# Kernel tuning notes

Hardware: AMD Instinct MI355X
Metric: run time of the kernel (lower is better)

The kernel has to match this reference:

```python
import jax, jax.numpy as jnp
import numpy as np

B, S, H = 32, 2048, 1024


def sparsemax(z, axis):
    # Martins & Astudillo (2016) sparsemax projection onto the simplex.
    n = z.shape[axis]
    z_sorted = -jnp.sort(-z, axis=axis)  # descending sort
    z_cum = jnp.cumsum(z_sorted, axis=axis)
    k = jnp.arange(1, n + 1, dtype=z.dtype).reshape(
        [n if i == (axis % z.ndim) else 1 for i in range(z.ndim)])
    support = (1.0 + k * z_sorted) > z_cum
    k_z = jnp.sum(support, axis=axis, keepdims=True)  # support size per row
    tau = (jnp.take_along_axis(z_cum, k_z.astype(jnp.int32) - 1, axis=axis) - 1.0) / k_z.astype(z.dtype)
    return jnp.maximum(z - tau, 0.0)


def setup_inputs() -> dict:
    key = jax.random.key(0)
    ks = jax.random.split(key, 8)
    s = 1.0 / np.sqrt(H)
    return {
        "encoder_output": jax.random.normal(ks[0], (B, S, H), jnp.float32),
        "decoder_hidden": jax.random.normal(ks[1], (B, H), jnp.float32),
        "Wa_w": jax.random.uniform(ks[2], (H, H), jnp.float32, -s, s),
        "Wa_b": jax.random.uniform(ks[3], (H,), jnp.float32, -s, s),
        "Ua_w": jax.random.uniform(ks[4], (H, H), jnp.float32, -s, s),
        "Ua_b": jax.random.uniform(ks[5], (H,), jnp.float32, -s, s),
        "Va_w": jax.random.uniform(ks[6], (1, H), jnp.float32, -s, s),
        "Va_b": jax.random.uniform(ks[7], (1,), jnp.float32, -s, s),
    }


def reference(encoder_output, decoder_hidden, Wa_w, Wa_b, Ua_w, Ua_b, Va_w, Va_b):
    # query: [B, 1, H]
    query = (decoder_hidden @ Wa_w.T + Wa_b)[:, None, :]
    # keys: [B, S, H]
    keys = jnp.einsum('bsh,oh->bso', encoder_output, Ua_w) + Ua_b
    # energy: [B, S]
    energy = jnp.einsum('bsh,h->bs', jnp.tanh(keys + query), Va_w[0]) + Va_b[0]
    attention_weights = sparsemax(energy, axis=1)  # [B, S]
    # context: [B, 1, H]
    context = jnp.einsum('bs,bsh->bh', attention_weights, encoder_output)[:, None, :]
    return (context, attention_weights)
```

## Files before the change

kernel.cpp:

```cpp
#include <hip/hip_runtime.h>
#include <stdint.h>
#include <stddef.h>

#define BB 32
#define SS 2048
#define HH 1024
#define MTOT (BB*SS)
#define NC 16

typedef _Float16 h8 __attribute__((ext_vector_type(8)));
typedef float f32x4 __attribute__((ext_vector_type(4)));

__device__ __forceinline__ void gload_lds16(const void* g, void* l) {
  __builtin_amdgcn_global_load_lds(
      (const __attribute__((address_space(1))) void*)g,
      (__attribute__((address_space(3))) void*)l,
      16, 0, 0);
}

__device__ __forceinline__ float fast_tanh(float x) {
  x = fminf(15.f, fmaxf(-15.f, x));
  float t = __expf(2.f * x);
  return (t - 1.f) * __builtin_amdgcn_rcpf(t + 1.f);
}

__global__ __launch_bounds__(256) void cvt_h(const float* __restrict__ src,
                                             _Float16* __restrict__ dst) {
  int t = blockIdx.x * 256 + threadIdx.x;
  const float4* s4 = (const float4*)src + (size_t)t * 2;
  float4 f0 = s4[0], f1 = s4[1];
  h8 v;
  v[0]=(_Float16)f0.x; v[1]=(_Float16)f0.y; v[2]=(_Float16)f0.z; v[3]=(_Float16)f0.w;
  v[4]=(_Float16)f1.x; v[5]=(_Float16)f1.y; v[6]=(_Float16)f1.z; v[7]=(_Float16)f1.w;
  *(h8*)(dst + (size_t)t * 8) = v;
}

__global__ __launch_bounds__(256) void query_k(const float* __restrict__ dh,
                                               const float* __restrict__ Wa,
                                               const float* __restrict__ Wa_b,
                                               const float* __restrict__ Ua_b,
                                               float* __restrict__ qv) {
  int gw = (blockIdx.x * 256 + threadIdx.x) >> 6;
  int lane = threadIdx.x & 63;
  int o = gw >> 5;
  int b = gw & 31;
  const float4* x4 = (const float4*)(dh + (size_t)b * HH);
  const float4* w4 = (const float4*)(Wa + (size_t)o * HH);
  float s = 0.f;
#pragma unroll
  for (int j = 0; j < 4; ++j) {
    float4 a = x4[lane + 64 * j];
    float4 c = w4[lane + 64 * j];
    s += a.x * c.x + a.y * c.y + a.z * c.z + a.w * c.w;
  }
#pragma unroll
  for (int d = 32; d >= 1; d >>= 1) s += __shfl_xor(s, d, 64);
  if (lane == 0) qv[b * HH + o] = s + Wa_b[o] + Ua_b[o];
}

template<bool AH>
__global__ __launch_bounds__(256) void energy_gemm(const float* __restrict__ Ag,
                                                   const _Float16* __restrict__ Ahp,
                                                   const _Float16* __restrict__ Bh,
                                                   const float* __restrict__ qv,
                                                   const float* __restrict__ Va,
                                                   float* __restrict__ energy) {
  __shared__ __align__(16) _Float16 As[128 * 64];
  __shared__ __align__(16) _Float16 Bs[128 * 64];

  const int tid  = threadIdx.x;
  const int lane = tid & 63;
  const int w    = tid >> 6;
  const int wrow = (w & 1) * 64;
  const int wcol = (w >> 1) * 64;
  const int lr   = lane & 15;
  const int lq   = lane >> 4;

  const int x     = blockIdx.x;
  const int xcd   = x & 7;
  const int i6    = x >> 3;
  const int strip = xcd * 64 + (i6 >> 3);
  const int nblk  = i6 & 7;
  const int m0    = strip * 128;
  const int n0    = nblk * 128;

  f32x4 acc[4][4];
#pragma unroll
  for (int i = 0; i < 4; ++i)
#pragma unroll
    for (int j = 0; j < 4; ++j) acc[i][j] = (f32x4){0.f, 0.f, 0.f, 0.f};

  for (int kt = 0; kt < 16; ++kt) {
    const int k0 = kt * 64;
#pragma unroll
    for (int i = 0; i < 4; ++i) {
      int g = tid + 256 * i;
      int r = g >> 3;
      int c = (g & 7) ^ (r & 7);
      gload_lds16(Bh + (size_t)(n0 + r) * HH + k0 + c * 8, &Bs[g * 8]);
    }
    if constexpr (AH) {
#pragma unroll
      for (int i = 0; i < 4; ++i) {
        int g = tid + 256 * i;
        int r = g >> 3;
        int c = (g & 7) ^ (r & 7);
        gload_lds16(Ahp + (size_t)(m0 + r) * HH + k0 + c * 8, &As[g * 8]);
      }
    } else {
      float4 fa[8];
#pragma unroll
      for (int i = 0; i < 4; ++i) {
        int g = tid + 256 * i;
        int r = g >> 3;
        int c = (g & 7) ^ (r & 7);
        const float* src = Ag + (size_t)(m0 + r) * HH + k0 + c * 8;
        fa[2 * i]     = *(const float4*)src;
        fa[2 * i + 1] = *(const float4*)(src + 4);
      }
#pragma unroll
      for (int i = 0; i < 4; ++i) {
        int g = tid + 256 * i;
        h8 v;
        v[0]=(_Float16)fa[2*i].x;   v[1]=(_Float16)fa[2*i].y;
        v[2]=(_Float16)fa[2*i].z;   v[3]=(_Float16)fa[2*i].w;
        v[4]=(_Float16)fa[2*i+1].x; v[5]=(_Float16)fa[2*i+1].y;
        v[6]=(_Float16)fa[2*i+1].z; v[7]=(_Float16)fa[2*i+1].w;
        *(h8*)&As[g * 8] = v;
      }
    }
    __syncthreads();
#pragma unroll
    for (int kk = 0; kk < 2; ++kk) {
      h8 af[4], bf[4];
#pragma unroll
      for (int i = 0; i < 4; ++i) {
        int ra = wrow + i * 16 + lr;
        int ca = kk * 4 + lq;
        af[i] = *(const h8*)&As[(ra * 8 + (ca ^ (ra & 7))) * 8];
        int rb = wcol + i * 16 + lr;
        bf[i] = *(const h8*)&Bs[(rb * 8 + (ca ^ (rb & 7))) * 8];
      }
#pragma unroll
      for (int i = 0; i < 4; ++i)
#pragma unroll
        for (int j = 0; j < 4; ++j)
          acc[i][j] = __builtin_amdgcn_mfma_f32_16x16x32_f16(af[i], bf[j], acc[i][j], 0, 0, 0);
    }
    __syncthreads();
  }

  const int bq = m0 >> 11;
  float qvv[4], vaw[4];
#pragma unroll
  for (int j = 0; j < 4; ++j) {
    int n = n0 + wcol + j * 16 + lr;
    qvv[j] = qv[bq * HH + n];
    vaw[j] = Va[n];
  }
#pragma unroll
  for (int i = 0; i < 4; ++i) {
    float p[4] = {0.f, 0.f, 0.f, 0.f};
#pragma unroll
    for (int j = 0; j < 4; ++j)
#pragma unroll
      for (int r = 0; r < 4; ++r)
        p[r] += fast_tanh(acc[i][j][r] + qvv[j]) * vaw[j];
#pragma unroll
    for (int r = 0; r < 4; ++r) {
      float v = p[r];
      v += __shfl_xor(v, 1, 64);
      v += __shfl_xor(v, 2, 64);
      v += __shfl_xor(v, 4, 64);
      v += __shfl_xor(v, 8, 64);
      if (lr == 0) {
        int m = m0 + wrow + i * 16 + lq * 4 + r;
        atomicAdd(&energy[m], v);
      }
    }
  }
}

__global__ __launch_bounds__(256) void sparse_k(const float* __restrict__ energy,
                                                const float* __restrict__ Va_b,
                                                float* __restrict__ attn,
                                                int* __restrict__ scnt,
                                                int* __restrict__ ssidx,
                                                float* __restrict__ saval) {
  const int b = blockIdx.x;
  const int tid = threadIdx.x;
  const int lane = tid & 63;
  const int w = tid >> 6;
  __shared__ int cnt;
  if (tid == 0) cnt = 0;

  const float* z = energy + (size_t)b * SS;
  const float vb = Va_b[0];
  float zv[32];
#pragma unroll
  for (int k = 0; k < 32; ++k) zv[k] = z[lane + 64 * k] + vb;

  float mx = zv[0];
#pragma unroll
  for (int k = 1; k < 32; ++k) mx = fmaxf(mx, zv[k]);
#pragma unroll
  for (int d = 32; d >= 1; d >>= 1) mx = fmaxf(mx, __shfl_xor(mx, d, 64));

  float lo = mx - 1.f, hi = mx;
  for (int it = 0; it < 40; ++it) {
    float tau = 0.5f * (lo + hi);
    float ss = 0.f;
#pragma unroll
    for (int k = 0; k < 32; ++k) ss += fmaxf(zv[k] - tau, 0.f);
#pragma unroll
    for (int d = 32; d >= 1; d >>= 1) ss += __shfl_xor(ss, d, 64);
    if (ss >= 1.f) lo = tau; else hi = tau;
  }
  const float tau = 0.5f * (lo + hi);

  __syncthreads();
  int* si = ssidx + b * SS;
  float* av = saval + b * SS;
#pragma unroll
  for (int kk = 0; kk < 8; ++kk) {
    int k = w * 8 + kk;
    int s = lane + 64 * k;
    float a = fmaxf(zv[k] - tau, 0.f);
    attn[(size_t)b * SS + s] = a;
    if (a > 0.f) {
      int p = atomicAdd(&cnt, 1);
      si[p] = s;
      av[p] = a;
    }
  }
  __syncthreads();
  if (tid == 0) scnt[b] = cnt;
}

__global__ __launch_bounds__(256) void ctx_k(const float* __restrict__ enc,
                                             const int* __restrict__ scnt,
                                             const int* __restrict__ ssidx,
                                             const float* __restrict__ saval,
                                             float* __restrict__ ctx) {
  const int b = blockIdx.x >> 4;
  const int c = blockIdx.x & (NC - 1);
  const int tid = threadIdx.x;
  const int n = scnt[b];
  if (c >= n) return;

  const float* eb = enc + (size_t)b * SS * HH;
  const int* si = ssidx + b * SS;
  const float* av = saval + b * SS;

  float c0 = 0.f, c1 = 0.f, c2 = 0.f, c3 = 0.f;
  for (int p = c; p < n; p += NC) {
    float a = av[p];
    const float* row = eb + (size_t)si[p] * HH;
    c0 += a * row[tid];
    c1 += a * row[tid + 256];
    c2 += a * row[tid + 512];
    c3 += a * row[tid + 768];
  }
  atomicAdd(&ctx[(size_t)b * HH + tid],       c0);
  atomicAdd(&ctx[(size_t)b * HH + tid + 256], c1);
  atomicAdd(&ctx[(size_t)b * HH + tid + 512], c2);
  atomicAdd(&ctx[(size_t)b * HH + tid + 768], c3);
}

extern "C" void kernel_launch(void* const* d_in, const int* in_sizes, int n_in,
                              void* d_out, int out_size, void* d_ws, size_t ws_size,
                              hipStream_t stream) {
  const float* enc  = (const float*)d_in[0];
  const float* dh   = (const float*)d_in[1];
  const float* Wa_w = (const float*)d_in[2];
  const float* Wa_b = (const float*)d_in[3];
  const float* Ua_w = (const float*)d_in[4];
  const float* Ua_b = (const float*)d_in[5];
  const float* Va_w = (const float*)d_in[6];
  const float* Va_b = (const float*)d_in[7];

  float* out_ctx  = (float*)d_out;
  float* out_attn = (float*)d_out + BB * HH;

  char* ws = (char*)d_ws;
  _Float16* Ua_h = (_Float16*)ws;
  float* qv      = (float*)(ws + 2 * 1024 * 1024);
  float* energy  = (float*)(ws + 2 * 1024 * 1024 + 128 * 1024);
  int*   scnt    = (int*)  (ws + 2 * 1024 * 1024 + 512 * 1024);
  int*   ssidx   = (int*)  (ws + 2 * 1024 * 1024 + 516 * 1024);
  float* saval   = (float*)(ws + 2 * 1024 * 1024 + 772 * 1024);
  _Float16* enc_h = (_Float16*)(ws + 4 * 1024 * 1024);

  const size_t need_h = 4ull * 1024 * 1024 + (size_t)MTOT * HH * sizeof(_Float16);
  const bool use_ah = (ws_size >= need_h);

  if (use_ah) {
    cvt_h<<<32768, 256, 0, stream>>>(enc, enc_h);
  }
  cvt_h<<<512, 256, 0, stream>>>(Ua_w, Ua_h);
  query_k<<<8192, 256, 0, stream>>>(dh, Wa_w, Wa_b, Ua_b, qv);
  hipMemsetAsync(energy, 0, MTOT * sizeof(float), stream);
  hipMemsetAsync(out_ctx, 0, BB * HH * sizeof(float), stream);
  if (use_ah) {
    energy_gemm<true><<<4096, 256, 0, stream>>>(enc, enc_h, Ua_h, qv, Va_w, energy);
  } else {
    energy_gemm<false><<<4096, 256, 0, stream>>>(enc, nullptr, Ua_h, qv, Va_w, energy);
  }
  sparse_k<<<BB, 256, 0, stream>>>(energy, Va_b, out_attn, scnt, ssidx, saval);
  ctx_k<<<BB * NC, 256, 0, stream>>>(enc, scnt, ssidx, saval, out_ctx);
}
```

Measured before the change: 642.6 us.

## Double-buffer LDS in fp16 energy GEMM and batch conversion kernel work

Splits the energy GEMM into separate fp16 and fp32 kernels and gives the fp16 path double-buffered LDS. The global-to-LDS loads for the next K tile are issued before the MFMAs on the current tile, with one barrier per iteration instead of two, so load latency can hide behind compute. The encoder conversion kernel now processes eight chunks per thread with a smaller grid, cutting launch and scheduling overhead. The doubled LDS (64 KB per block) may lower occupancy. With only one barrier, a new stage's writes to a buffer are not separated from slower waves' reads of that buffer, which risks a race.

```diff
diff --git a/kernel.cpp b/kernel.cpp
--- a/kernel.cpp
+++ b/kernel.cpp
@@ -33,6 +33,20 @@
   v[0]=(_Float16)f0.x; v[1]=(_Float16)f0.y; v[2]=(_Float16)f0.z; v[3]=(_Float16)f0.w;
   v[4]=(_Float16)f1.x; v[5]=(_Float16)f1.y; v[6]=(_Float16)f1.z; v[7]=(_Float16)f1.w;
   *(h8*)(dst + (size_t)t * 8) = v;
+}
+
+__global__ __launch_bounds__(256) void cvt_h_big(const float* __restrict__ src,
+                                                 _Float16* __restrict__ dst) {
+#pragma unroll
+  for (int i = 0; i < 8; ++i) {
+    size_t t = ((size_t)(blockIdx.x + 4096 * i)) * 256 + threadIdx.x;
+    const float4* s4 = (const float4*)src + t * 2;
+    float4 f0 = s4[0], f1 = s4[1];
+    h8 v;
+    v[0]=(_Float16)f0.x; v[1]=(_Float16)f0.y; v[2]=(_Float16)f0.z; v[3]=(_Float16)f0.w;
+    v[4]=(_Float16)f1.x; v[5]=(_Float16)f1.y; v[6]=(_Float16)f1.z; v[7]=(_Float16)f1.w;
+    *(h8*)(dst + t * 8) = v;
+  }
 }
 
 __global__ __launch_bounds__(256) void query_k(const float* __restrict__ dh,
@@ -58,15 +72,13 @@
   if (lane == 0) qv[b * HH + o] = s + Wa_b[o] + Ua_b[o];
 }
 
-template<bool AH>
-__global__ __launch_bounds__(256) void energy_gemm(const float* __restrict__ Ag,
-                                                   const _Float16* __restrict__ Ahp,
-                                                   const _Float16* __restrict__ Bh,
-                                                   const float* __restrict__ qv,
-                                                   const float* __restrict__ Va,
-                                                   float* __restrict__ energy) {
-  __shared__ __align__(16) _Float16 As[128 * 64];
-  __shared__ __align__(16) _Float16 Bs[128 * 64];
+__global__ __launch_bounds__(256) void energy_gemm_h(const _Float16* __restrict__ Ahp,
+                                                     const _Float16* __restrict__ Bh,
+                                                     const float* __restrict__ qv,
+                                                     const float* __restrict__ Va,
+                                                     float* __restrict__ energy) {
+  __shared__ __align__(16) _Float16 As[2][128 * 64];
+  __shared__ __align__(16) _Float16 Bs[2][128 * 64];
 
   const int tid  = threadIdx.x;
   const int lane = tid & 63;
@@ -90,6 +102,105 @@
 #pragma unroll
     for (int j = 0; j < 4; ++j) acc[i][j] = (f32x4){0.f, 0.f, 0.f, 0.f};
 
+#define STAGE(buf, kt_) do {                                                   \
+    const int k0_ = (kt_) * 64;                                                \
+    _Pragma("unroll")                                                          \
+    for (int i_ = 0; i_ < 4; ++i_) {                                           \
+      int g_ = tid + 256 * i_;                                                 \
+      int r_ = g_ >> 3;                                                        \
+      int c_ = (g_ & 7) ^ (r_ & 7);                                            \
+      gload_lds16(Bh + (size_t)(n0 + r_) * HH + k0_ + c_ * 8,                  \
+                  &Bs[buf][g_ * 8]);                                           \
+      gload_lds16(Ahp + (size_t)(m0 + r_) * HH + k0_ + c_ * 8,                 \
+                  &As[buf][g_ * 8]);                                           \
+    }                                                                          \
+  } while (0)
+
+  STAGE(0, 0);
+  __syncthreads();
+  int cur = 0;
+
+  for (int kt = 0; kt < 16; ++kt) {
+    if (kt + 1 < 16) STAGE(cur ^ 1, kt + 1);
+#pragma unroll
+    for (int kk = 0; kk < 2; ++kk) {
+      h8 af[4], bf[4];
+#pragma unroll
+      for (int i = 0; i < 4; ++i) {
+        int ra = wrow + i * 16 + lr;
+        int ca = kk * 4 + lq;
+        af[i] = *(const h8*)&As[cur][(ra * 8 + (ca ^ (ra & 7))) * 8];
+        int rb = wcol + i * 16 + lr;
+        bf[i] = *(const h8*)&Bs[cur][(rb * 8 + (ca ^ (rb & 7))) * 8];
+      }
+#pragma unroll
+      for (int i = 0; i < 4; ++i)
+#pragma unroll
+        for (int j = 0; j < 4; ++j)
+          acc[i][j] = __builtin_amdgcn_mfma_f32_16x16x32_f16(af[i], bf[j], acc[i][j], 0, 0, 0);
+    }
+    __syncthreads();
+    cur ^= 1;
+  }
+#undef STAGE
+
+  const int bq = m0 >> 11;
+  float qvv[4], vaw[4];
+#pragma unroll
+  for (int j = 0; j < 4; ++j) {
+    int n = n0 + wcol + j * 16 + lr;
+    qvv[j] = qv[bq * HH + n];
+    vaw[j] = Va[n];
+  }
+#pragma unroll
+  for (int i = 0; i < 4; ++i) {
+    float p[4] = {0.f, 0.f, 0.f, 0.f};
+#pragma unroll
+    for (int j = 0; j < 4; ++j)
+#pragma unroll
+      for (int r = 0; r < 4; ++r)
+        p[r] += fast_tanh(acc[i][j][r] + qvv[j]) * vaw[j];
+#pragma unroll
+    for (int r = 0; r < 4; ++r) {
+      float v = p[r];
+      v += __shfl_xor(v, 1, 64);
+      v += __shfl_xor(v, 2, 64);
+      v += __shfl_xor(v, 4, 64);
+      v += __shfl_xor(v, 8, 64);
+      if (lr == 0) {
+        int m = m0 + wrow + i * 16 + lq * 4 + r;
+        atomicAdd(&energy[m], v);
+      }
+    }
+  }
+}
+
+__global__ __launch_bounds__(256) void energy_gemm_f32(const float* __restrict__ Ag,
+                                                       const _Float16* __restrict__ Bh,
+                                                       const float* __restrict__ qv,
+                                                       const float* __restrict__ Va,
+                                                       float* __restrict__ energy) {
+  __shared__ __align__(16) _Float16 As[128 * 64];
+  __shared__ __align__(16) _Float16 Bs[128 * 64];
+  const int tid  = threadIdx.x;
+  const int lane = tid & 63;
+  const int w    = tid >> 6;
+  const int wrow = (w & 1) * 64;
+  const int wcol = (w >> 1) * 64;
+  const int lr   = lane & 15;
+  const int lq   = lane >> 4;
+  const int x     = blockIdx.x;
+  const int xcd   = x & 7;
+  const int i6    = x >> 3;
+  const int strip = xcd * 64 + (i6 >> 3);
+  const int nblk  = i6 & 7;
+  const int m0    = strip * 128;
+  const int n0    = nblk * 128;
+  f32x4 acc[4][4];
+#pragma unroll
+  for (int i = 0; i < 4; ++i)
+#pragma unroll
+    for (int j = 0; j < 4; ++j) acc[i][j] = (f32x4){0.f, 0.f, 0.f, 0.f};
   for (int kt = 0; kt < 16; ++kt) {
     const int k0 = kt * 64;
 #pragma unroll
@@ -99,35 +210,25 @@
       int c = (g & 7) ^ (r & 7);
       gload_lds16(Bh + (size_t)(n0 + r) * HH + k0 + c * 8, &Bs[g * 8]);
     }
-    if constexpr (AH) {
-#pragma unroll
-      for (int i = 0; i < 4; ++i) {
-        int g = tid + 256 * i;
-        int r = g >> 3;
-        int c = (g & 7) ^ (r & 7);
-        gload_lds16(Ahp + (size_t)(m0 + r) * HH + k0 + c * 8, &As[g * 8]);
-      }
-    } else {
-      float4 fa[8];
-#pragma unroll
-      for (int i = 0; i < 4; ++i) {
-        int g = tid + 256 * i;
-        int r = g >> 3;
-        int c = (g & 7) ^ (r & 7);
-        const float* src = Ag + (size_t)(m0 + r) * HH + k0 + c * 8;
-        fa[2 * i]     = *(const float4*)src;
-        fa[2 * i + 1] = *(const float4*)(src + 4);
-      }
-#pragma unroll
-      for (int i = 0; i < 4; ++i) {
-        int g = tid + 256 * i;
-        h8 v;
-        v[0]=(_Float16)fa[2*i].x;   v[1]=(_Float16)fa[2*i].y;
-        v[2]=(_Float16)fa[2*i].z;   v[3]=(_Float16)fa[2*i].w;
-        v[4]=(_Float16)fa[2*i+1].x; v[5]=(_Float16)fa[2*i+1].y;
-        v[6]=(_Float16)fa[2*i+1].z; v[7]=(_Float16)fa[2*i+1].w;
-        *(h8*)&As[g * 8] = v;
-      }
+    float4 fa[8];
+#pragma unroll
+    for (int i = 0; i < 4; ++i) {
+      int g = tid + 256 * i;
+      int r = g >> 3;
+      int c = (g & 7) ^ (r & 7);
+      const float* src = Ag + (size_t)(m0 + r) * HH + k0 + c * 8;
+      fa[2 * i]     = *(const float4*)src;
+      fa[2 * i + 1] = *(const float4*)(src + 4);
+    }
+#pragma unroll
+    for (int i = 0; i < 4; ++i) {
+      int g = tid + 256 * i;
+      h8 v;
+      v[0]=(_Float16)fa[2*i].x;   v[1]=(_Float16)fa[2*i].y;
+      v[2]=(_Float16)fa[2*i].z;   v[3]=(_Float16)fa[2*i].w;
+      v[4]=(_Float16)fa[2*i+1].x; v[5]=(_Float16)fa[2*i+1].y;
+      v[6]=(_Float16)fa[2*i+1].z; v[7]=(_Float16)fa[2*i+1].w;
+      *(h8*)&As[g * 8] = v;
     }
     __syncthreads();
 #pragma unroll
@@ -149,7 +250,6 @@
     }
     __syncthreads();
   }
-
   const int bq = m0 >> 11;
   float qvv[4], vaw[4];
 #pragma unroll
@@ -295,16 +395,16 @@
   const bool use_ah = (ws_size >= need_h);
 
   if (use_ah) {
-    cvt_h<<<32768, 256, 0, stream>>>(enc, enc_h);
+    cvt_h_big<<<4096, 256, 0, stream>>>(enc, enc_h);
   }
   cvt_h<<<512, 256, 0, stream>>>(Ua_w, Ua_h);
   query_k<<<8192, 256, 0, stream>>>(dh, Wa_w, Wa_b, Ua_b, qv);
   hipMemsetAsync(energy, 0, MTOT * sizeof(float), stream);
   hipMemsetAsync(out_ctx, 0, BB * HH * sizeof(float), stream);
   if (use_ah) {
-    energy_gemm<true><<<4096, 256, 0, stream>>>(enc, enc_h, Ua_h, qv, Va_w, energy);
+    energy_gemm_h<<<4096, 256, 0, stream>>>(enc_h, Ua_h, qv, Va_w, energy);
   } else {
-    energy_gemm<false><<<4096, 256, 0, stream>>>(enc, nullptr, Ua_h, qv, Va_w, energy);
+    energy_gemm_f32<<<4096, 256, 0, stream>>>(enc, Ua_h, qv, Va_w, energy);
   }
   sparse_k<<<BB, 256, 0, stream>>>(energy, Va_b, out_attn, scnt, ssidx, saval);
   ctx_k<<<BB * NC, 256, 0, stream>>>(enc, scnt, ssidx, saval, out_ctx);
```

Result: slower. 674.7 us (+5.0%).
